# Kernel optimization log

Measured on AMD Instinct MI355X. Metric: run time of the kernel, lower is better.

Reference implementation:

```python
import jax, jax.numpy as jnp
import numpy as np
from jax import lax

B, T, D = 4, 1024, 512      # batch, seq_len, d_model
L = 4                        # n_layers
N = 16                       # d_state
DC = 4                       # d_conv
DI = 2 * D                   # d_inner = expand * d_model
DTR = D // 16                # dt_rank
H = 128                      # head hidden dim
EPS = 1e-5


def layer_norm(x, g, b):
    mu = jnp.mean(x, axis=-1, keepdims=True)
    var = jnp.mean((x - mu) ** 2, axis=-1, keepdims=True)
    return (x - mu) * lax.rsqrt(var + EPS) * g + b


def setup_inputs() -> dict:
    key = jax.random.key(0)
    ks = jax.random.split(key, 24)
    s = 0.02
    return {
        "daily_summaries": jax.random.normal(ks[0], (B, T, D), jnp.float32),
        # per-layer mamba params, stacked on leading L axis
        "in_proj_w": s * jax.random.normal(ks[1], (L, 2 * DI, D), jnp.float32),
        "conv_w": s * jax.random.normal(ks[2], (L, DI, DC), jnp.float32),
        "conv_b": jnp.zeros((L, DI), jnp.float32),
        "x_proj_w": s * jax.random.normal(ks[3], (L, DTR + 2 * N, DI), jnp.float32),
        "dt_proj_w": s * jax.random.normal(ks[4], (L, DI, DTR), jnp.float32),
        "dt_proj_b": jnp.full((L, DI), -4.0, jnp.float32),  # softplus -> small dt
        "A_log": jnp.log(jnp.broadcast_to(jnp.arange(1, N + 1, dtype=jnp.float32), (L, DI, N))),
        "D_skip": jnp.ones((L, DI), jnp.float32),
        "out_proj_w": s * jax.random.normal(ks[5], (L, D, DI), jnp.float32),
        "ln_g": jnp.ones((L, D), jnp.float32),
        "ln_b": jnp.zeros((L, D), jnp.float32),
        # attention pooling
        "attn_w": s * jax.random.normal(ks[6], (1, D), jnp.float32),
        "attn_b": jnp.zeros((1,), jnp.float32),
        # VIX head
        "h1_w": s * jax.random.normal(ks[7], (H, D), jnp.float32),
        "h1_b": jnp.zeros((H,), jnp.float32),
        "ln1_g": jnp.ones((H,), jnp.float32),
        "ln1_b": jnp.zeros((H,), jnp.float32),
        "h2_w": s * jax.random.normal(ks[8], (H, H), jnp.float32),
        "h2_b": jnp.zeros((H,), jnp.float32),
        "ln2_g": jnp.ones((H,), jnp.float32),
        "ln2_b": jnp.zeros((H,), jnp.float32),
        # note: torch zero-inits the final layer; we use random so grads are nonzero
        "h3_w": s * jax.random.normal(ks[9], (1, H), jnp.float32),
        "h3_b": jnp.zeros((1,), jnp.float32),
    }


def mamba_layer(x, in_w, cw, cb, xp_w, dt_w, dt_b, A_log, D_skip, out_w):
    """x: [B,T,D] -> [B,T,D]; canonical Mamba selective scan."""
    xz = jnp.einsum('btd,ed->bte', x, in_w)          # [B,T,2*DI]
    x_in, z = jnp.split(xz, 2, axis=-1)
    # causal depthwise conv over time
    xc = lax.conv_general_dilated(
        x_in.transpose(0, 2, 1), cw[:, None, :], (1,), [(DC - 1, 0)],
        feature_group_count=DI, dimension_numbers=('NCH', 'OIH', 'NCH'))
    xc = jax.nn.silu(xc + cb[None, :, None]).transpose(0, 2, 1)   # [B,T,DI]
    dbc = jnp.einsum('btd,ed->bte', xc, xp_w)        # [B,T,DTR+2N]
    dt_r, Bm, Cm = dbc[..., :DTR], dbc[..., DTR:DTR + N], dbc[..., DTR + N:]
    dt = jax.nn.softplus(jnp.einsum('btr,dr->btd', dt_r, dt_w) + dt_b)  # [B,T,DI]
    A = -jnp.exp(A_log)                              # [DI,N]
    dA = jnp.exp(dt[..., None] * A)                  # [B,T,DI,N]
    dBx = dt[..., None] * Bm[:, :, None, :] * xc[..., None]  # [B,T,DI,N]

    def step(h, inp):
        dA_t, dBx_t, C_t = inp
        h = dA_t * h + dBx_t                         # [B,DI,N]
        return h, jnp.einsum('bdn,bn->bd', h, C_t)

    h0 = jnp.zeros((x.shape[0], DI, N), x.dtype)
    _, ys = lax.scan(step, h0, (dA.transpose(1, 0, 2, 3),
                                dBx.transpose(1, 0, 2, 3),
                                Cm.transpose(1, 0, 2)))
    y = ys.transpose(1, 0, 2) + xc * D_skip          # [B,T,DI]
    y = y * jax.nn.silu(z)
    return jnp.einsum('btd,ed->bte', y, out_w)       # [B,T,D]


def reference(daily_summaries, in_proj_w, conv_w, conv_b, x_proj_w, dt_proj_w,
              dt_proj_b, A_log, D_skip, out_proj_w, ln_g, ln_b, attn_w, attn_b,
              h1_w, h1_b, ln1_g, ln1_b, h2_w, h2_b, ln2_g, ln2_b, h3_w, h3_b):
    x = daily_summaries  # proj is Identity (d_model_l1 == d_model)
    for l in range(L):
        residual = x
        y = mamba_layer(x, in_proj_w[l], conv_w[l], conv_b[l], x_proj_w[l],
                        dt_proj_w[l], dt_proj_b[l], A_log[l], D_skip[l], out_proj_w[l])
        x = layer_norm(y, ln_g[l], ln_b[l]) + residual
    # attention pooling (no mask)
    scores = jnp.einsum('btd,od->bto', x, attn_w) + attn_b   # [B,T,1]
    w = jax.nn.softmax(scores, axis=1)
    pooled = jnp.sum(w * x, axis=1)                          # [B,D]
    # VIX head: Linear -> LN -> GELU (x2) -> Linear
    h1 = jax.nn.gelu(layer_norm(pooled @ h1_w.T + h1_b, ln1_g, ln1_b), approximate=False)
    h2 = jax.nn.gelu(layer_norm(h1 @ h2_w.T + h2_b, ln2_g, ln2_b), approximate=False)
    return (h2 @ h3_w.T + h3_b).squeeze(-1)                  # [B]
```

## Files before the change

kernel.cpp:

```cpp
#include <hip/hip_runtime.h>
#include <hip/hip_bf16.h>
#include <math.h>

#define BATCH 4
#define TLEN 1024
#define DMODEL 512
#define DINNER 1024
#define NSTATE 16
#define EPSV 1e-5f
#define NC 32
#define CT 32
#define DSTR 36
#define LOG2E 1.44269504088896f

typedef __attribute__((ext_vector_type(8))) short bf16x8;
typedef __attribute__((ext_vector_type(4))) float f32x4;

__device__ inline unsigned short f2bf(float f) {
  union { float f; unsigned int u; } c; c.f = f;
  unsigned int u = c.u;
  return (unsigned short)((u + 0x7FFFu + ((u >> 16) & 1u)) >> 16);
}

__device__ inline float warpReduceSum(float v) {
#pragma unroll
  for (int o = 32; o > 0; o >>= 1) v += __shfl_down(v, o, 64);
  return v;
}
__device__ inline float warpReduceMax(float v) {
#pragma unroll
  for (int o = 32; o > 0; o >>= 1) v = fmaxf(v, __shfl_down(v, o, 64));
  return v;
}
__device__ inline float2 blockReduceSum2_256(float a, float b) {
  __shared__ float sma[4], smb[4];
  int lane = threadIdx.x & 63, wid = threadIdx.x >> 6;
#pragma unroll
  for (int o = 32; o > 0; o >>= 1) { a += __shfl_down(a, o, 64); b += __shfl_down(b, o, 64); }
  if (lane == 0) { sma[wid] = a; smb[wid] = b; }
  __syncthreads();
  float ra = sma[0] + sma[1] + sma[2] + sma[3];
  float rb = smb[0] + smb[1] + smb[2] + smb[3];
  __syncthreads();
  return make_float2(ra, rb);
}
__device__ inline float blockReduceSum256(float v) {
  __shared__ float sm[4];
  int lane = threadIdx.x & 63, wid = threadIdx.x >> 6;
  v = warpReduceSum(v);
  if (lane == 0) sm[wid] = v;
  __syncthreads();
  float r = sm[0] + sm[1] + sm[2] + sm[3];
  __syncthreads();
  return r;
}
__device__ inline float blockReduceMax256(float v) {
  __shared__ float sm[4];
  int lane = threadIdx.x & 63, wid = threadIdx.x >> 6;
  v = warpReduceMax(v);
  if (lane == 0) sm[wid] = v;
  __syncthreads();
  float r = fmaxf(fmaxf(sm[0], sm[1]), fmaxf(sm[2], sm[3]));
  __syncthreads();
  return r;
}
__device__ inline float blockReduceSum128(float v) {
  __shared__ float sm[2];
  int lane = threadIdx.x & 63, wid = threadIdx.x >> 6;
  v = warpReduceSum(v);
  if (lane == 0) sm[wid] = v;
  __syncthreads();
  float r = sm[0] + sm[1];
  __syncthreads();
  return r;
}

__global__ void __launch_bounds__(256)
cast_f32_bf16(const float* __restrict__ src, unsigned short* __restrict__ dst, int n) {
  int i = (blockIdx.x * 256 + threadIdx.x) * 4;
  if (i >= n) return;
  float4 v = *(const float4*)(src + i);
  dst[i + 0] = f2bf(v.x);
  dst[i + 1] = f2bf(v.y);
  dst[i + 2] = f2bf(v.z);
  dst[i + 3] = f2bf(v.w);
}

#define LDP 72
__global__ void __launch_bounds__(256)
gemm_bf16(const unsigned short* __restrict__ A, int lda,
          const unsigned short* __restrict__ B, int ldb,
          float* __restrict__ C, int ldc, int K) {
  __shared__ unsigned short As[128 * LDP];
  __shared__ unsigned short Bs[128 * LDP];
  const int tid = threadIdx.x;
  const int lane = tid & 63, wid = tid >> 6;
  const int wm = wid >> 1, wn = wid & 1;
  const int row0 = blockIdx.y * 128, col0 = blockIdx.x * 128;
  const int c8 = (tid & 7) * 8;
  const int r0 = tid >> 3;
  const int l15 = lane & 15, lq = lane >> 4;
  f32x4 acc[4][4] = {};
  for (int k0 = 0; k0 < K; k0 += 64) {
#pragma unroll
    for (int p = 0; p < 4; p++) {
      int row = r0 + p * 32;
      bf16x8 av = *(const bf16x8*)(A + (size_t)(row0 + row) * lda + k0 + c8);
      bf16x8 bv = *(const bf16x8*)(B + (size_t)(col0 + row) * ldb + k0 + c8);
      *(bf16x8*)(As + row * LDP + c8) = av;
      *(bf16x8*)(Bs + row * LDP + c8) = bv;
    }
    __syncthreads();
#pragma unroll
    for (int s = 0; s < 2; s++) {
      const int koff = s * 32 + lq * 8;
      bf16x8 af[4], bfr[4];
#pragma unroll
      for (int i = 0; i < 4; i++)
        af[i] = *(const bf16x8*)(As + (wm * 64 + i * 16 + l15) * LDP + koff);
#pragma unroll
      for (int j = 0; j < 4; j++)
        bfr[j] = *(const bf16x8*)(Bs + (wn * 64 + j * 16 + l15) * LDP + koff);
#pragma unroll
      for (int i = 0; i < 4; i++)
#pragma unroll
        for (int j = 0; j < 4; j++)
          acc[i][j] = __builtin_amdgcn_mfma_f32_16x16x32_bf16(af[i], bfr[j], acc[i][j], 0, 0, 0);
    }
    __syncthreads();
  }
#pragma unroll
  for (int i = 0; i < 4; i++) {
#pragma unroll
    for (int j = 0; j < 4; j++) {
#pragma unroll
      for (int r = 0; r < 4; r++) {
        int row = row0 + wm * 64 + i * 16 + lq * 4 + r;
        int col = col0 + wn * 64 + j * 16 + l15;
        C[(size_t)row * ldc + col] = acc[i][j][r];
      }
    }
  }
}

__global__ void __launch_bounds__(256)
gemm_bf16_n64(const unsigned short* __restrict__ A, int lda,
              const unsigned short* __restrict__ B, int ldb,
              float* __restrict__ C, int ldc, int K) {
  __shared__ unsigned short As[128 * LDP];
  __shared__ unsigned short Bs[64 * LDP];
  const int tid = threadIdx.x;
  const int lane = tid & 63, wid = tid >> 6;
  const int wm = wid >> 1, wn = wid & 1;
  const int row0 = blockIdx.y * 128, col0 = blockIdx.x * 64;
  const int c8 = (tid & 7) * 8;
  const int r0 = tid >> 3;
  const int l15 = lane & 15, lq = lane >> 4;
  f32x4 acc[4][2] = {};
  for (int k0 = 0; k0 < K; k0 += 64) {
#pragma unroll
    for (int p = 0; p < 4; p++) {
      int row = r0 + p * 32;
      bf16x8 av = *(const bf16x8*)(A + (size_t)(row0 + row) * lda + k0 + c8);
      *(bf16x8*)(As + row * LDP + c8) = av;
    }
#pragma unroll
    for (int p = 0; p < 2; p++) {
      int row = r0 + p * 32;
      bf16x8 bv = *(const bf16x8*)(B + (size_t)(col0 + row) * ldb + k0 + c8);
      *(bf16x8*)(Bs + row * LDP + c8) = bv;
    }
    __syncthreads();
#pragma unroll
    for (int s = 0; s < 2; s++) {
      const int koff = s * 32 + lq * 8;
      bf16x8 af[4], bfr[2];
#pragma unroll
      for (int i = 0; i < 4; i++)
        af[i] = *(const bf16x8*)(As + (wm * 64 + i * 16 + l15) * LDP + koff);
#pragma unroll
      for (int j = 0; j < 2; j++)
        bfr[j] = *(const bf16x8*)(Bs + (wn * 32 + j * 16 + l15) * LDP + koff);
#pragma unroll
      for (int i = 0; i < 4; i++)
#pragma unroll
        for (int j = 0; j < 2; j++)
          acc[i][j] = __builtin_amdgcn_mfma_f32_16x16x32_bf16(af[i], bfr[j], acc[i][j], 0, 0, 0);
    }
    __syncthreads();
  }
#pragma unroll
  for (int i = 0; i < 4; i++) {
#pragma unroll
    for (int j = 0; j < 2; j++) {
#pragma unroll
      for (int r = 0; r < 4; r++) {
        int row = row0 + wm * 64 + i * 16 + lq * 4 + r;
        int col = col0 + wn * 32 + j * 16 + l15;
        C[(size_t)row * ldc + col] = acc[i][j][r];
      }
    }
  }
}

template <int EPI>
__global__ void __launch_bounds__(256)
gemm_atb(const float* __restrict__ A, int lda,
         const float* __restrict__ B, int ldb,
         float* __restrict__ C, int ldc,
         int K, const float* __restrict__ bias) {
  __shared__ __align__(16) float As[16][68];
  __shared__ __align__(16) float Bs[16][68];
  const int tid = threadIdx.x;
  const int tx = tid & 15, ty = tid >> 4;
  const int row0 = blockIdx.y * 64, col0 = blockIdx.x * 64;
  float acc[4][4] = {};
  for (int k0 = 0; k0 < K; k0 += 16) {
#pragma unroll
    for (int i = 0; i < 4; i++) {
      int e = tid + i * 256;
      int m = e >> 4, kk = e & 15;
      As[kk][m] = A[(size_t)(row0 + m) * lda + k0 + kk];
      Bs[kk][m] = B[(size_t)(col0 + m) * ldb + k0 + kk];
    }
    __syncthreads();
#pragma unroll
    for (int kk = 0; kk < 16; kk++) {
      float4 a4 = *(const float4*)&As[kk][ty << 2];
      float4 b4 = *(const float4*)&Bs[kk][tx << 2];
      float a[4] = {a4.x, a4.y, a4.z, a4.w};
      float b[4] = {b4.x, b4.y, b4.z, b4.w};
#pragma unroll
      for (int i = 0; i < 4; i++)
#pragma unroll
        for (int j = 0; j < 4; j++) acc[i][j] = fmaf(a[i], b[j], acc[i][j]);
    }
    __syncthreads();
  }
#pragma unroll
  for (int i = 0; i < 4; i++) {
    size_t r = row0 + (ty << 2) + i;
#pragma unroll
    for (int j = 0; j < 4; j++) {
      int c = col0 + (tx << 2) + j;
      float v = acc[i][j];
      if (EPI == 1) {
        v += bias[c];
        v = (v > 20.f) ? v : log1pf(__expf(v));
      }
      C[r * ldc + c] = v;
    }
  }
}

__global__ void __launch_bounds__(256)
gemm_atb_sk(const float* __restrict__ A, int lda,
            const float* __restrict__ B, int ldb,
            float* __restrict__ Cpart, int ldc, int KCH) {
  __shared__ __align__(16) float As[16][68];
  __shared__ __align__(16) float Bs[16][68];
  const int tid = threadIdx.x;
  const int tx = tid & 15, ty = tid >> 4;
  const int row0 = blockIdx.y * 64, col0 = blockIdx.x * 64;
  const int kbase = blockIdx.z * KCH;
  float* Cz = Cpart + (size_t)blockIdx.z * 4096 * 64;
  float acc[4][4] = {};
  for (int k0 = 0; k0 < KCH; k0 += 16) {
#pragma unroll
    for (int i = 0; i < 4; i++) {
      int e = tid + i * 256;
      int m = e >> 4, kk = e & 15;
      As[kk][m] = A[(size_t)(row0 + m) * lda + kbase + k0 + kk];
      Bs[kk][m] = B[(size_t)(col0 + m) * ldb + kbase + k0 + kk];
    }
    __syncthreads();
#pragma unroll
    for (int kk = 0; kk < 16; kk++) {
      float4 a4 = *(const float4*)&As[kk][ty << 2];
      float4 b4 = *(const float4*)&Bs[kk][tx << 2];
      float a[4] = {a4.x, a4.y, a4.z, a4.w};
      float b[4] = {b4.x, b4.y, b4.z, b4.w};
#pragma unroll
      for (int i = 0; i < 4; i++)
#pragma unroll
        for (int j = 0; j < 4; j++) acc[i][j] = fmaf(a[i], b[j], acc[i][j]);
    }
    __syncthreads();
  }
#pragma unroll
  for (int i = 0; i < 4; i++) {
    size_t r = row0 + (ty << 2) + i;
#pragma unroll
    for (int j = 0; j < 4; j++) {
      int c = col0 + (tx << 2) + j;
      Cz[r * ldc + c] = acc[i][j];
    }
  }
}

__global__ void __launch_bounds__(256)
reduce4_kernel(const float* __restrict__ part, float* __restrict__ out, int n) {
  int i = (blockIdx.x * 256 + threadIdx.x) * 4;
  if (i >= n) return;
  float4 a = *(const float4*)(part + i);
  float4 b = *(const float4*)(part + n + i);
  float4 c = *(const float4*)(part + 2 * n + i);
  float4 d = *(const float4*)(part + 3 * n + i);
  float4 r;
  r.x = a.x + b.x + c.x + d.x;
  r.y = a.y + b.y + c.y + d.y;
  r.z = a.z + b.z + c.z + d.z;
  r.w = a.w + b.w + c.w + d.w;
  *(float4*)(out + i) = r;
}

__global__ void conv_silu_kernel(const float* __restrict__ xz,
                                 const float* __restrict__ cw,
                                 const float* __restrict__ cb,
                                 float* __restrict__ xc) {
  int idx = blockIdx.x * 256 + threadIdx.x;
  int d = idx & 1023;
  int bt = idx >> 10;
  int t = bt & 1023;
  float acc = cb[d];
  const float* w = cw + d * 4;
#pragma unroll
  for (int k = 0; k < 4; k++) {
    int ts = t - 3 + k;
    if (ts >= 0) acc = fmaf(xz[((size_t)bt + (ts - t)) * 2048 + d], w[k], acc);
  }
  float sig = 1.f / (1.f + __expf(-acc));
  xc[idx] = acc * sig;
}

__global__ void __launch_bounds__(256)
scan_part1(const float* __restrict__ dt, const float* __restrict__ xc,
           const float* __restrict__ dbc, const float* __restrict__ A_log,
           float* __restrict__ hloc, float* __restrict__ sdtb) {
  __shared__ float dts[64 * DSTR];
  __shared__ float xcs[64 * DSTR];
  __shared__ float Bsh[CT * 20];
  const int chunk = blockIdx.x, dg = blockIdx.y, b = blockIdx.z;
  const int tid = threadIdx.x;
  const int ch = tid >> 2, q4 = (tid & 3) * 4;
  const int d = dg * 64 + ch;
  const size_t bt0 = (size_t)b * TLEN + chunk * CT;
  for (int i = tid; i < CT * 64; i += 256) {
    int t = i >> 6, c = i & 63;
    size_t bt = bt0 + t;
    dts[c * DSTR + t] = dt[bt * 1024 + dg * 64 + c];
    xcs[c * DSTR + t] = xc[bt * 1024 + dg * 64 + c];
  }
  for (int i = tid; i < CT * 16; i += 256) {
    int t = i >> 4, n = i & 15;
    Bsh[t * 20 + n] = dbc[(bt0 + t) * 64 + 32 + n];
  }
  __syncthreads();
  float4 al = *(const float4*)&A_log[d * 16 + q4];
  float4 A;
  A.x = -__expf(al.x) * LOG2E; A.y = -__expf(al.y) * LOG2E;
  A.z = -__expf(al.z) * LOG2E; A.w = -__expf(al.w) * LOG2E;
  float4 h = {0.f, 0.f, 0.f, 0.f};
  float sdt = 0.f;
#pragma unroll
  for (int t0 = 0; t0 < CT; t0 += 4) {
    float4 dt4 = *(const float4*)&dts[ch * DSTR + t0];
    float4 xc4 = *(const float4*)&xcs[ch * DSTR + t0];
    const float dta[4] = {dt4.x, dt4.y, dt4.z, dt4.w};
    const float xca[4] = {xc4.x, xc4.y, xc4.z, xc4.w};
#pragma unroll
    for (int u = 0; u < 4; u++) {
      float dtv = dta[u];
      float4 B4 = *(const float4*)&Bsh[(t0 + u) * 20 + q4];
      float uin = dtv * xca[u];
      h.x = fmaf(exp2f(dtv * A.x), h.x, uin * B4.x);
      h.y = fmaf(exp2f(dtv * A.y), h.y, uin * B4.y);
      h.z = fmaf(exp2f(dtv * A.z), h.z, uin * B4.z);
      h.w = fmaf(exp2f(dtv * A.w), h.w, uin * B4.w);
      sdt += dtv;
    }
  }
  size_t slab = (size_t)(b * 16 + dg);
  *(float4*)&hloc[(slab * NC + chunk) * 1024 + tid * 4] = h;
  sdtb[(slab * NC + chunk) * 256 + tid] = sdt;
}

__global__ void __launch_bounds__(256)
scan_part2(const float* __restrict__ dt, const float* __restrict__ xc,
           const float* __restrict__ dbc, const float* __restrict__ xz,
           const float* __restrict__ A_log, const float* __restrict__ Dsk,
           const float* __restrict__ hloc, const float* __restrict__ sdtb,
           unsigned short* __restrict__ ybf) {
  __shared__ float dts[64 * DSTR];
  __shared__ float xcs[64 * DSTR];
  __shared__ float Bsh[CT * 20];
  __shared__ float Csh[CT * 20];
  __shared__ float ys[CT * 64];
  const int chunk = blockIdx.x, dg = blockIdx.y, b = blockIdx.z;
  const int tid = threadIdx.x;
  const int q = tid & 3;
  const int ch = tid >> 2, q4 = q * 4;
  const int d = dg * 64 + ch;
  const size_t bt0 = (size_t)b * TLEN + chunk * CT;
  float4 al = *(const float4*)&A_log[d * 16 + q4];
  float4 A;
  A.x = -__expf(al.x) * LOG2E; A.y = -__expf(al.y) * LOG2E;
  A.z = -__expf(al.z) * LOG2E; A.w = -__expf(al.w) * LOG2E;
  float4 h = {0.f, 0.f, 0.f, 0.f};
  {
    size_t slab = (size_t)(b * 16 + dg);
    const f32x4* hl4 = (const f32x4*)&hloc[slab * NC * 1024];
    const float* sd = &sdtb[slab * NC * 256 + tid];
    int c = 0;
    for (; c + 4 <= chunk; c += 4) {
      f32x4 hl[4];
      float s[4];
#pragma unroll
      for (int j = 0; j < 4; j++) {
        hl[j] = hl4[(size_t)(c + j) * 256 + tid];
        s[j] = sd[(size_t)(c + j) * 256];
      }
#pragma unroll
      for (int j = 0; j < 4; j++) {
        h.x = fmaf(exp2f(s[j] * A.x), h.x, hl[j][0]);
        h.y = fmaf(exp2f(s[j] * A.y), h.y, hl[j][1]);
        h.z = fmaf(exp2f(s[j] * A.z), h.z, hl[j][2]);
        h.w = fmaf(exp2f(s[j] * A.w), h.w, hl[j][3]);
      }
    }
    for (; c < chunk; c++) {
      f32x4 hl = hl4[(size_t)c * 256 + tid];
      float s = sd[(size_t)c * 256];
      h.x = fmaf(exp2f(s * A.x), h.x, hl[0]);
      h.y = fmaf(exp2f(s * A.y), h.y, hl[1]);
      h.z = fmaf(exp2f(s * A.z), h.z, hl[2]);
      h.w = fmaf(exp2f(s * A.w), h.w, hl[3]);
    }
  }
  for (int i = tid; i < CT * 64; i += 256) {
    int t = i >> 6, c = i & 63;
    size_t bt = bt0 + t;
    dts[c * DSTR + t] = dt[bt * 1024 + dg * 64 + c];
    xcs[c * DSTR + t] = xc[bt * 1024 + dg * 64 + c];
  }
  for (int i = tid; i < CT * 16; i += 256) {
    int t = i >> 4, n = i & 15;
    Bsh[t * 20 + n] = dbc[(bt0 + t) * 64 + 32 + n];
    Csh[t * 20 + n] = dbc[(bt0 + t) * 64 + 48 + n];
  }
  __syncthreads();
  const float Dv = Dsk[d];
#pragma unroll
  for (int t0 = 0; t0 < CT; t0 += 4) {
    float4 dt4 = *(const float4*)&dts[ch * DSTR + t0];
    float4 xc4 = *(const float4*)&xcs[ch * DSTR + t0];
    const float dta[4] = {dt4.x, dt4.y, dt4.z, dt4.w};
    const float xca[4] = {xc4.x, xc4.y, xc4.z, xc4.w};
#pragma unroll
    for (int u = 0; u < 4; u++) {
      float dtv = dta[u];
      float4 B4 = *(const float4*)&Bsh[(t0 + u) * 20 + q4];
      float4 C4 = *(const float4*)&Csh[(t0 + u) * 20 + q4];
      float uin = dtv * xca[u];
      h.x = fmaf(exp2f(dtv * A.x), h.x, uin * B4.x);
      h.y = fmaf(exp2f(dtv * A.y), h.y, uin * B4.y);
      h.z = fmaf(exp2f(dtv * A.z), h.z, uin * B4.z);
      h.w = fmaf(exp2f(dtv * A.w), h.w, uin * B4.w);
      float cs = h.x * C4.x + h.y * C4.y + h.z * C4.z + h.w * C4.w;
      cs += __shfl_xor(cs, 1, 4);
      cs += __shfl_xor(cs, 2, 4);
      if (q == 0) ys[(t0 + u) * 64 + ch] = cs + xca[u] * Dv;
    }
  }
  __syncthreads();
  for (int i = tid; i < CT * 64; i += 256) {
    int t = i >> 6, c = i & 63;
    size_t bt = bt0 + t;
    float zv = xz[bt * 2048 + 1024 + dg * 64 + c];
    float sig = 1.f / (1.f + __expf(-zv));
    ybf[bt * 1024 + dg * 64 + c] = f2bf(ys[t * 64 + c] * (zv * sig));
  }
}

__global__ void __launch_bounds__(256)
ln_res_kernel(const float* __restrict__ mo, const float* __restrict__ res,
              const float* __restrict__ g, const float* __restrict__ bb,
              float* __restrict__ xout, unsigned short* __restrict__ xout_bf) {
  int row = blockIdx.x;
  int tid = threadIdx.x;
  size_t base = (size_t)row * 512;
  float v0 = mo[base + tid], v1 = mo[base + tid + 256];
  float2 ss = blockReduceSum2_256(v0 + v1, v0 * v0 + v1 * v1);
  float mu = ss.x * (1.f / 512.f);
  float var = ss.y * (1.f / 512.f) - mu * mu;
  float rs = rsqrtf(var + EPSV);
  float o0 = (v0 - mu) * rs * g[tid] + bb[tid] + res[base + tid];
  float o1 = (v1 - mu) * rs * g[tid + 256] + bb[tid + 256] + res[base + tid + 256];
  xout[base + tid] = o0;
  xout[base + tid + 256] = o1;
  xout_bf[base + tid] = f2bf(o0);
  xout_bf[base + tid + 256] = f2bf(o1);
}

__global__ void __launch_bounds__(256)
score_kernel(const float* __restrict__ x, const float* __restrict__ aw,
             const float* __restrict__ ab, float* __restrict__ sc) {
  int row = blockIdx.x * 4 + (threadIdx.x >> 6);
  int lane = threadIdx.x & 63;
  size_t base = (size_t)row * 512;
  float p = 0.f;
#pragma unroll
  for (int j = 0; j < 8; j++) p = fmaf(x[base + lane + 64 * j], aw[lane + 64 * j], p);
  p = warpReduceSum(p);
  if (lane == 0) sc[row] = p + ab[0];
}

__global__ void __launch_bounds__(256)
softmax_t_kernel(const float* __restrict__ sc, float* __restrict__ wsm) {
  int b = blockIdx.x, tid = threadIdx.x;
  float v[4];
  float m = -INFINITY;
#pragma unroll
  for (int j = 0; j < 4; j++) { v[j] = sc[b * 1024 + tid + 256 * j]; m = fmaxf(m, v[j]); }
  m = blockReduceMax256(m);
  float s = 0.f;
#pragma unroll
  for (int j = 0; j < 4; j++) { v[j] = __expf(v[j] - m); s += v[j]; }
  s = blockReduceSum256(s);
  float inv = 1.f / s;
#pragma unroll
  for (int j = 0; j < 4; j++) wsm[b * 1024 + tid + 256 * j] = v[j] * inv;
}

__global__ void __launch_bounds__(256)
pool_partial(const float* __restrict__ x, const float* __restrict__ wsm,
             float* __restrict__ partial) {
  int tc = blockIdx.x, b = blockIdx.y, tid = threadIdx.x;
  float a0 = 0.f, a1 = 0.f;
  for (int t = tc * 32; t < tc * 32 + 32; t++) {
    float wv = wsm[b * 1024 + t];
    size_t base = ((size_t)b * 1024 + t) * 512;
    a0 = fmaf(wv, x[base + tid], a0);
    a1 = fmaf(wv, x[base + tid + 256], a1);
  }
  size_t pb = ((size_t)b * 32 + tc) * 512;
  partial[pb + tid] = a0;
  partial[pb + tid + 256] = a1;
}

__global__ void __launch_bounds__(256)
pool_reduce(const float* __restrict__ partial, float* __restrict__ pooled) {
  int b = blockIdx.x, tid = threadIdx.x;
  float a0 = 0.f, a1 = 0.f;
  for (int tc = 0; tc < 32; tc++) {
    size_t pb = ((size_t)b * 32 + tc) * 512;
    a0 += partial[pb + tid];
    a1 += partial[pb + tid + 256];
  }
  pooled[b * 512 + tid] = a0;
  pooled[b * 512 + tid + 256] = a1;
}

__device__ inline float gelu_exact(float x) {
  return 0.5f * x * (1.f + erff(x * 0.70710678118654752f));
}
__global__ void __launch_bounds__(128)
head_kernel(const float* __restrict__ pooled,
            const float* __restrict__ h1w, const float* __restrict__ h1b,
            const float* __restrict__ g1, const float* __restrict__ b1,
            const float* __restrict__ h2w, const float* __restrict__ h2b,
            const float* __restrict__ g2, const float* __restrict__ b2,
            const float* __restrict__ h3w, const float* __restrict__ h3b,
            float* __restrict__ out) {
  int tid = threadIdx.x;
  int b = blockIdx.x;
  __shared__ float hs[128];
  float s = h1b[tid];
  const float* p = pooled + b * 512;
  for (int d = 0; d < 512; d += 4) {
    float4 pv = *(const float4*)(p + d);
    float4 wv = *(const float4*)(h1w + tid * 512 + d);
    s = fmaf(pv.x, wv.x, s); s = fmaf(pv.y, wv.y, s);
    s = fmaf(pv.z, wv.z, s); s = fmaf(pv.w, wv.w, s);
  }
  float mu = blockReduceSum128(s) * (1.f / 128.f);
  float dd = s - mu;
  float var = blockReduceSum128(dd * dd) * (1.f / 128.f);
  float v = dd * rsqrtf(var + EPSV) * g1[tid] + b1[tid];
  hs[tid] = gelu_exact(v);
  __syncthreads();
  float s2 = h2b[tid];
  for (int j = 0; j < 128; j++) s2 = fmaf(hs[j], h2w[tid * 128 + j], s2);
  float mu2 = blockReduceSum128(s2) * (1.f / 128.f);
  float d2 = s2 - mu2;
  float var2 = blockReduceSum128(d2 * d2) * (1.f / 128.f);
  float v2 = d2 * rsqrtf(var2 + EPSV) * g2[tid] + b2[tid];
  float h2v = gelu_exact(v2);
  float o = blockReduceSum128(h2v * h3w[tid]);
  if (tid == 0) out[b] = o + h3b[0];
}

extern "C" void kernel_launch(void* const* d_in, const int* in_sizes, int n_in,
                              void* d_out, int out_size, void* d_ws, size_t ws_size,
                              hipStream_t stream) {
  (void)in_sizes; (void)n_in; (void)out_size; (void)ws_size;
  const float* x0   = (const float*)d_in[0];
  const float* inw  = (const float*)d_in[1];
  const float* cw   = (const float*)d_in[2];
  const float* cb   = (const float*)d_in[3];
  const float* xpw  = (const float*)d_in[4];
  const float* dtw  = (const float*)d_in[5];
  const float* dtb  = (const float*)d_in[6];
  const float* alog = (const float*)d_in[7];
  const float* dsk  = (const float*)d_in[8];
  const float* outw = (const float*)d_in[9];
  const float* lng  = (const float*)d_in[10];
  const float* lnb  = (const float*)d_in[11];
  const float* aw   = (const float*)d_in[12];
  const float* ab   = (const float*)d_in[13];
  const float* h1w  = (const float*)d_in[14];
  const float* h1b  = (const float*)d_in[15];
  const float* g1   = (const float*)d_in[16];
  const float* b1   = (const float*)d_in[17];
  const float* h2w  = (const float*)d_in[18];
  const float* h2b  = (const float*)d_in[19];
  const float* g2   = (const float*)d_in[20];
  const float* b2   = (const float*)d_in[21];
  const float* h3w  = (const float*)d_in[22];
  const float* h3b  = (const float*)d_in[23];

  float* ws = (float*)d_ws;
  float* xz      = ws;
  float* xc      = xz + 8388608;
  float* dbc     = xc + 4194304;
  float* dt      = dbc + 262144;
  float* mo      = dt + 4194304;
  float* xbuf    = mo + 2097152;
  float* scores  = xbuf + 2097152;
  float* wsm     = scores + 4096;
  float* partial = wsm + 4096;
  float* pooled  = partial + 65536;
  unsigned short* abuf    = (unsigned short*)(pooled + 2048);
  unsigned short* ybf     = abuf + 2097152;
  unsigned short* wbf_in  = ybf + 4194304;
  unsigned short* wbf_out = wbf_in + 4194304;
  float* xpart = (float*)(wbf_out + 2097152);
  float* hloc = mo;
  float* sdtb = xpart;

  cast_f32_bf16<<<4096, 256, 0, stream>>>(inw, wbf_in, 4194304);
  cast_f32_bf16<<<2048, 256, 0, stream>>>(outw, wbf_out, 2097152);
  cast_f32_bf16<<<2048, 256, 0, stream>>>(x0, abuf, 2097152);

  const float* xcur = x0;
  for (int l = 0; l < 4; l++) {
    gemm_bf16<<<dim3(16, 32), 256, 0, stream>>>(
        abuf, 512, wbf_in + (size_t)l * 2048 * 512, 512, xz, 2048, 512);
    conv_silu_kernel<<<16384, 256, 0, stream>>>(xz, cw + l * 4096, cb + l * 1024, xc);
    gemm_atb_sk<<<dim3(1, 64, 4), 256, 0, stream>>>(
        xc, 1024, xpw + (size_t)l * 64 * 1024, 1024, xpart, 64, 256);
    reduce4_kernel<<<256, 256, 0, stream>>>(xpart, dbc, 262144);
    gemm_atb<1><<<dim3(16, 64), 256, 0, stream>>>(
        dbc, 64, dtw + (size_t)l * 1024 * 32, 32, dt, 1024, 32, dtb + l * 1024);
    scan_part1<<<dim3(NC, 16, 4), 256, 0, stream>>>(
        dt, xc, dbc, alog + (size_t)l * 16384, hloc, sdtb);
    scan_part2<<<dim3(NC, 16, 4), 256, 0, stream>>>(
        dt, xc, dbc, xz, alog + (size_t)l * 16384, dsk + l * 1024,
        hloc, sdtb, ybf);
    gemm_bf16_n64<<<dim3(8, 32), 256, 0, stream>>>(
        ybf, 1024, wbf_out + (size_t)l * 512 * 1024, 1024, mo, 512, 1024);
    ln_res_kernel<<<4096, 256, 0, stream>>>(mo, xcur, lng + l * 512, lnb + l * 512,
                                            xbuf, abuf);
    xcur = xbuf;
  }
  score_kernel<<<1024, 256, 0, stream>>>(xbuf, aw, ab, scores);
  softmax_t_kernel<<<4, 256, 0, stream>>>(scores, wsm);
  pool_partial<<<dim3(32, 4), 256, 0, stream>>>(xbuf, wsm, partial);
  pool_reduce<<<4, 256, 0, stream>>>(partial, pooled);
  head_kernel<<<4, 128, 0, stream>>>(pooled, h1w, h1b, g1, b1, h2w, h2b, g2, b2,
                                     h3w, h3b, (float*)d_out);
}
```

Baseline: 841.9 us.

## Store intermediates in bf16, MFMA x_proj, and add separate scan prefix kernel

Splits the in_proj output into an fp32 x half and a bf16 z half, and stores conv output and dt in bf16 to cut memory traffic for the scan kernels. The x_proj matmul moves from a split-K fp32 SIMT GEMM plus reduce onto the bf16 MFMA GEMM. A new scan_prefix kernel computes each chunk's initial state once, replacing the redundant per-block serial prefix inside scan_part2. This lowers precision of dt, xc and z to bf16 and adds one launch per layer.

```diff
diff --git a/kernel.cpp b/kernel.cpp
--- a/kernel.cpp
+++ b/kernel.cpp
@@ -21,6 +21,11 @@
   unsigned int u = c.u;
   return (unsigned short)((u + 0x7FFFu + ((u >> 16) & 1u)) >> 16);
 }
+__device__ inline float bf2f(unsigned short u) {
+  union { unsigned int i; float f; } c;
+  c.i = ((unsigned int)u) << 16;
+  return c.f;
+}
 
 __device__ inline float warpReduceSum(float v) {
 #pragma unroll
@@ -88,9 +93,9 @@
 
 #define LDP 72
 __global__ void __launch_bounds__(256)
-gemm_bf16(const unsigned short* __restrict__ A, int lda,
-          const unsigned short* __restrict__ B, int ldb,
-          float* __restrict__ C, int ldc, int K) {
+gemm_bf16_split(const unsigned short* __restrict__ A, int lda,
+                const unsigned short* __restrict__ B, int ldb,
+                float* __restrict__ Cx, unsigned short* __restrict__ Cz, int K) {
   __shared__ unsigned short As[128 * LDP];
   __shared__ unsigned short Bs[128 * LDP];
   const int tid = threadIdx.x;
@@ -129,17 +134,28 @@
     }
     __syncthreads();
   }
-#pragma unroll
-  for (int i = 0; i < 4; i++) {
-#pragma unroll
-    for (int j = 0; j < 4; j++) {
-#pragma unroll
-      for (int r = 0; r < 4; r++) {
-        int row = row0 + wm * 64 + i * 16 + lq * 4 + r;
-        int col = col0 + wn * 64 + j * 16 + l15;
-        C[(size_t)row * ldc + col] = acc[i][j][r];
-      }
-    }
+  if (col0 < 1024) {
+#pragma unroll
+    for (int i = 0; i < 4; i++)
+#pragma unroll
+      for (int j = 0; j < 4; j++)
+#pragma unroll
+        for (int r = 0; r < 4; r++) {
+          int row = row0 + wm * 64 + i * 16 + lq * 4 + r;
+          int col = col0 + wn * 64 + j * 16 + l15;
+          Cx[(size_t)row * 1024 + col] = acc[i][j][r];
+        }
+  } else {
+#pragma unroll
+    for (int i = 0; i < 4; i++)
+#pragma unroll
+      for (int j = 0; j < 4; j++)
+#pragma unroll
+        for (int r = 0; r < 4; r++) {
+          int row = row0 + wm * 64 + i * 16 + lq * 4 + r;
+          int col = col0 - 1024 + wn * 64 + j * 16 + l15;
+          Cz[(size_t)row * 1024 + col] = f2bf(acc[i][j][r]);
+        }
   }
 }
 
@@ -190,38 +206,33 @@
     __syncthreads();
   }
 #pragma unroll
-  for (int i = 0; i < 4; i++) {
-#pragma unroll
-    for (int j = 0; j < 2; j++) {
+  for (int i = 0; i < 4; i++)
+#pragma unroll
+    for (int j = 0; j < 2; j++)
 #pragma unroll
       for (int r = 0; r < 4; r++) {
         int row = row0 + wm * 64 + i * 16 + lq * 4 + r;
         int col = col0 + wn * 32 + j * 16 + l15;
         C[(size_t)row * ldc + col] = acc[i][j][r];
       }
-    }
-  }
-}
-
-template <int EPI>
-__global__ void __launch_bounds__(256)
-gemm_atb(const float* __restrict__ A, int lda,
-         const float* __restrict__ B, int ldb,
-         float* __restrict__ C, int ldc,
-         int K, const float* __restrict__ bias) {
+}
+
+__global__ void __launch_bounds__(256)
+gemm_dt(const float* __restrict__ A, const float* __restrict__ B,
+        unsigned short* __restrict__ C, const float* __restrict__ bias) {
   __shared__ __align__(16) float As[16][68];
   __shared__ __align__(16) float Bs[16][68];
   const int tid = threadIdx.x;
   const int tx = tid & 15, ty = tid >> 4;
   const int row0 = blockIdx.y * 64, col0 = blockIdx.x * 64;
   float acc[4][4] = {};
-  for (int k0 = 0; k0 < K; k0 += 16) {
+  for (int k0 = 0; k0 < 32; k0 += 16) {
 #pragma unroll
     for (int i = 0; i < 4; i++) {
       int e = tid + i * 256;
       int m = e >> 4, kk = e & 15;
-      As[kk][m] = A[(size_t)(row0 + m) * lda + k0 + kk];
-      Bs[kk][m] = B[(size_t)(col0 + m) * ldb + k0 + kk];
+      As[kk][m] = A[(size_t)(row0 + m) * 64 + k0 + kk];
+      Bs[kk][m] = B[(size_t)(col0 + m) * 32 + k0 + kk];
     }
     __syncthreads();
 #pragma unroll
@@ -243,81 +254,17 @@
 #pragma unroll
     for (int j = 0; j < 4; j++) {
       int c = col0 + (tx << 2) + j;
-      float v = acc[i][j];
-      if (EPI == 1) {
-        v += bias[c];
-        v = (v > 20.f) ? v : log1pf(__expf(v));
-      }
-      C[r * ldc + c] = v;
-    }
-  }
-}
-
-__global__ void __launch_bounds__(256)
-gemm_atb_sk(const float* __restrict__ A, int lda,
-            const float* __restrict__ B, int ldb,
-            float* __restrict__ Cpart, int ldc, int KCH) {
-  __shared__ __align__(16) float As[16][68];
-  __shared__ __align__(16) float Bs[16][68];
-  const int tid = threadIdx.x;
-  const int tx = tid & 15, ty = tid >> 4;
-  const int row0 = blockIdx.y * 64, col0 = blockIdx.x * 64;
-  const int kbase = blockIdx.z * KCH;
-  float* Cz = Cpart + (size_t)blockIdx.z * 4096 * 64;
-  float acc[4][4] = {};
-  for (int k0 = 0; k0 < KCH; k0 += 16) {
-#pragma unroll
-    for (int i = 0; i < 4; i++) {
-      int e = tid + i * 256;
-      int m = e >> 4, kk = e & 15;
-      As[kk][m] = A[(size_t)(row0 + m) * lda + kbase + k0 + kk];
-      Bs[kk][m] = B[(size_t)(col0 + m) * ldb + kbase + k0 + kk];
-    }
-    __syncthreads();
-#pragma unroll
-    for (int kk = 0; kk < 16; kk++) {
-      float4 a4 = *(const float4*)&As[kk][ty << 2];
-      float4 b4 = *(const float4*)&Bs[kk][tx << 2];
-      float a[4] = {a4.x, a4.y, a4.z, a4.w};
-      float b[4] = {b4.x, b4.y, b4.z, b4.w};
-#pragma unroll
-      for (int i = 0; i < 4; i++)
-#pragma unroll
-        for (int j = 0; j < 4; j++) acc[i][j] = fmaf(a[i], b[j], acc[i][j]);
-    }
-    __syncthreads();
-  }
-#pragma unroll
-  for (int i = 0; i < 4; i++) {
-    size_t r = row0 + (ty << 2) + i;
-#pragma unroll
-    for (int j = 0; j < 4; j++) {
-      int c = col0 + (tx << 2) + j;
-      Cz[r * ldc + c] = acc[i][j];
-    }
-  }
-}
-
-__global__ void __launch_bounds__(256)
-reduce4_kernel(const float* __restrict__ part, float* __restrict__ out, int n) {
-  int i = (blockIdx.x * 256 + threadIdx.x) * 4;
-  if (i >= n) return;
-  float4 a = *(const float4*)(part + i);
-  float4 b = *(const float4*)(part + n + i);
-  float4 c = *(const float4*)(part + 2 * n + i);
-  float4 d = *(const float4*)(part + 3 * n + i);
-  float4 r;
-  r.x = a.x + b.x + c.x + d.x;
-  r.y = a.y + b.y + c.y + d.y;
-  r.z = a.z + b.z + c.z + d.z;
-  r.w = a.w + b.w + c.w + d.w;
-  *(float4*)(out + i) = r;
-}
-
-__global__ void conv_silu_kernel(const float* __restrict__ xz,
+      float v = acc[i][j] + bias[c];
+      v = (v > 20.f) ? v : log1pf(__expf(v));
+      C[r * 1024 + c] = f2bf(v);
+    }
+  }
+}
+
+__global__ void conv_silu_kernel(const float* __restrict__ xin,
                                  const float* __restrict__ cw,
                                  const float* __restrict__ cb,
-                                 float* __restrict__ xc) {
+                                 unsigned short* __restrict__ xcbf) {
   int idx = blockIdx.x * 256 + threadIdx.x;
   int d = idx & 1023;
   int bt = idx >> 10;
@@ -327,18 +274,18 @@
 #pragma unroll
   for (int k = 0; k < 4; k++) {
     int ts = t - 3 + k;
-    if (ts >= 0) acc = fmaf(xz[((size_t)bt + (ts - t)) * 2048 + d], w[k], acc);
+    if (ts >= 0) acc = fmaf(xin[((size_t)bt + (ts - t)) * 1024 + d], w[k], acc);
   }
   float sig = 1.f / (1.f + __expf(-acc));
-  xc[idx] = acc * sig;
-}
-
-__global__ void __launch_bounds__(256)
-scan_part1(const float* __restrict__ dt, const float* __restrict__ xc,
+  xcbf[idx] = f2bf(acc * sig);
+}
+
+__global__ void __launch_bounds__(256)
+scan_part1(const unsigned short* __restrict__ dtbf, const unsigned short* __restrict__ xcbf,
            const float* __restrict__ dbc, const float* __restrict__ A_log,
            float* __restrict__ hloc, float* __restrict__ sdtb) {
-  __shared__ float dts[64 * DSTR];
-  __shared__ float xcs[64 * DSTR];
+  __shared__ unsigned short dts[64 * DSTR];
+  __shared__ unsigned short xcs[64 * DSTR];
   __shared__ float Bsh[CT * 20];
   const int chunk = blockIdx.x, dg = blockIdx.y, b = blockIdx.z;
   const int tid = threadIdx.x;
@@ -348,8 +295,8 @@
   for (int i = tid; i < CT * 64; i += 256) {
     int t = i >> 6, c = i & 63;
     size_t bt = bt0 + t;
-    dts[c * DSTR + t] = dt[bt * 1024 + dg * 64 + c];
-    xcs[c * DSTR + t] = xc[bt * 1024 + dg * 64 + c];
+    dts[c * DSTR + t] = dtbf[bt * 1024 + dg * 64 + c];
+    xcs[c * DSTR + t] = xcbf[bt * 1024 + dg * 64 + c];
   }
   for (int i = tid; i < CT * 16; i += 256) {
     int t = i >> 4, n = i & 15;
@@ -364,10 +311,10 @@
   float sdt = 0.f;
 #pragma unroll
   for (int t0 = 0; t0 < CT; t0 += 4) {
-    float4 dt4 = *(const float4*)&dts[ch * DSTR + t0];
-    float4 xc4 = *(const float4*)&xcs[ch * DSTR + t0];
-    const float dta[4] = {dt4.x, dt4.y, dt4.z, dt4.w};
-    const float xca[4] = {xc4.x, xc4.y, xc4.z, xc4.w};
+    ushort4 d4 = *(const ushort4*)&dts[ch * DSTR + t0];
+    ushort4 x4 = *(const ushort4*)&xcs[ch * DSTR + t0];
+    const float dta[4] = {bf2f(d4.x), bf2f(d4.y), bf2f(d4.z), bf2f(d4.w)};
+    const float xca[4] = {bf2f(x4.x), bf2f(x4.y), bf2f(x4.z), bf2f(x4.w)};
 #pragma unroll
     for (int u = 0; u < 4; u++) {
       float dtv = dta[u];
@@ -386,13 +333,37 @@
 }
 
 __global__ void __launch_bounds__(256)
-scan_part2(const float* __restrict__ dt, const float* __restrict__ xc,
-           const float* __restrict__ dbc, const float* __restrict__ xz,
+scan_prefix(const float* __restrict__ A_log, const float* __restrict__ hloc,
+            const float* __restrict__ sdtb, float* __restrict__ h0buf) {
+  const int slab = blockIdx.x;
+  const int tid = threadIdx.x;
+  const int dg = slab & 15;
+  const int ch = tid >> 2, q4 = (tid & 3) * 4;
+  const int d = dg * 64 + ch;
+  float4 al = *(const float4*)&A_log[d * 16 + q4];
+  float4 A;
+  A.x = -__expf(al.x) * LOG2E; A.y = -__expf(al.y) * LOG2E;
+  A.z = -__expf(al.z) * LOG2E; A.w = -__expf(al.w) * LOG2E;
+  float4 h = {0.f, 0.f, 0.f, 0.f};
+  size_t base = (size_t)slab * NC;
+  for (int c = 0; c < NC; c++) {
+    *(float4*)&h0buf[(base + c) * 1024 + tid * 4] = h;
+    float4 hl = *(const float4*)&hloc[(base + c) * 1024 + tid * 4];
+    float s = sdtb[(base + c) * 256 + tid];
+    h.x = fmaf(exp2f(s * A.x), h.x, hl.x);
+    h.y = fmaf(exp2f(s * A.y), h.y, hl.y);
+    h.z = fmaf(exp2f(s * A.z), h.z, hl.z);
+    h.w = fmaf(exp2f(s * A.w), h.w, hl.w);
+  }
+}
+
+__global__ void __launch_bounds__(256)
+scan_part2(const unsigned short* __restrict__ dtbf, const unsigned short* __restrict__ xcbf,
+           const float* __restrict__ dbc, const unsigned short* __restrict__ zbf,
            const float* __restrict__ A_log, const float* __restrict__ Dsk,
-           const float* __restrict__ hloc, const float* __restrict__ sdtb,
-           unsigned short* __restrict__ ybf) {
-  __shared__ float dts[64 * DSTR];
-  __shared__ float xcs[64 * DSTR];
+           const float* __restrict__ h0buf, unsigned short* __restrict__ ybf) {
+  __shared__ unsigned short dts[64 * DSTR];
+  __shared__ unsigned short xcs[64 * DSTR];
   __shared__ float Bsh[CT * 20];
   __shared__ float Csh[CT * 20];
   __shared__ float ys[CT * 64];
@@ -402,46 +373,17 @@
   const int ch = tid >> 2, q4 = q * 4;
   const int d = dg * 64 + ch;
   const size_t bt0 = (size_t)b * TLEN + chunk * CT;
+  const size_t slab = (size_t)(b * 16 + dg);
+  float4 h = *(const float4*)&h0buf[(slab * NC + chunk) * 1024 + tid * 4];
   float4 al = *(const float4*)&A_log[d * 16 + q4];
   float4 A;
   A.x = -__expf(al.x) * LOG2E; A.y = -__expf(al.y) * LOG2E;
   A.z = -__expf(al.z) * LOG2E; A.w = -__expf(al.w) * LOG2E;
-  float4 h = {0.f, 0.f, 0.f, 0.f};
-  {
-    size_t slab = (size_t)(b * 16 + dg);
-    const f32x4* hl4 = (const f32x4*)&hloc[slab * NC * 1024];
-    const float* sd = &sdtb[slab * NC * 256 + tid];
-    int c = 0;
-    for (; c + 4 <= chunk; c += 4) {
-      f32x4 hl[4];
-      float s[4];
-#pragma unroll
-      for (int j = 0; j < 4; j++) {
-        hl[j] = hl4[(size_t)(c + j) * 256 + tid];
-        s[j] = sd[(size_t)(c + j) * 256];
-      }
-#pragma unroll
-      for (int j = 0; j < 4; j++) {
-        h.x = fmaf(exp2f(s[j] * A.x), h.x, hl[j][0]);
-        h.y = fmaf(exp2f(s[j] * A.y), h.y, hl[j][1]);
-        h.z = fmaf(exp2f(s[j] * A.z), h.z, hl[j][2]);
-        h.w = fmaf(exp2f(s[j] * A.w), h.w, hl[j][3]);
-      }
-    }
-    for (; c < chunk; c++) {
-      f32x4 hl = hl4[(size_t)c * 256 + tid];
-      float s = sd[(size_t)c * 256];
-      h.x = fmaf(exp2f(s * A.x), h.x, hl[0]);
-      h.y = fmaf(exp2f(s * A.y), h.y, hl[1]);
-      h.z = fmaf(exp2f(s * A.z), h.z, hl[2]);
-      h.w = fmaf(exp2f(s * A.w), h.w, hl[3]);
-    }
-  }
   for (int i = tid; i < CT * 64; i += 256) {
     int t = i >> 6, c = i & 63;
     size_t bt = bt0 + t;
-    dts[c * DSTR + t] = dt[bt * 1024 + dg * 64 + c];
-    xcs[c * DSTR + t] = xc[bt * 1024 + dg * 64 + c];
+    dts[c * DSTR + t] = dtbf[bt * 1024 + dg * 64 + c];
+    xcs[c * DSTR + t] = xcbf[bt * 1024 + dg * 64 + c];
   }
   for (int i = tid; i < CT * 16; i += 256) {
     int t = i >> 4, n = i & 15;
@@ -452,10 +394,10 @@
   const float Dv = Dsk[d];
 #pragma unroll
   for (int t0 = 0; t0 < CT; t0 += 4) {
-    float4 dt4 = *(const float4*)&dts[ch * DSTR + t0];
-    float4 xc4 = *(const float4*)&xcs[ch * DSTR + t0];
-    const float dta[4] = {dt4.x, dt4.y, dt4.z, dt4.w};
-    const float xca[4] = {xc4.x, xc4.y, xc4.z, xc4.w};
+    ushort4 d4 = *(const ushort4*)&dts[ch * DSTR + t0];
+    ushort4 x4 = *(const ushort4*)&xcs[ch * DSTR + t0];
+    const float dta[4] = {bf2f(d4.x), bf2f(d4.y), bf2f(d4.z), bf2f(d4.w)};
+    const float xca[4] = {bf2f(x4.x), bf2f(x4.y), bf2f(x4.z), bf2f(x4.w)};
 #pragma unroll
     for (int u = 0; u < 4; u++) {
       float dtv = dta[u];
@@ -476,7 +418,7 @@
   for (int i = tid; i < CT * 64; i += 256) {
     int t = i >> 6, c = i & 63;
     size_t bt = bt0 + t;
-    float zv = xz[bt * 2048 + 1024 + dg * 64 + c];
+    float zv = bf2f(zbf[bt * 1024 + dg * 64 + c]);
     float sig = 1.f / (1.f + __expf(-zv));
     ybf[bt * 1024 + dg * 64 + c] = f2bf(ys[t * 64 + c] * (zv * sig));
   }
@@ -630,13 +572,17 @@
   const float* h3b  = (const float*)d_in[23];
 
   float* ws = (float*)d_ws;
-  float* xz      = ws;
-  float* xc      = xz + 8388608;
-  float* dbc     = xc + 4194304;
-  float* dt      = dbc + 262144;
-  float* mo      = dt + 4194304;
+  float* xin     = ws;
+  unsigned short* zbf  = (unsigned short*)(xin + 4194304);
+  unsigned short* xcbf = zbf + 4194304;
+  unsigned short* dtbf = xcbf + 4194304;
+  float* dbc     = (float*)(dtbf + 4194304);
+  float* mo      = dbc + 262144;
   float* xbuf    = mo + 2097152;
-  float* scores  = xbuf + 2097152;
+  float* hloc    = xbuf + 2097152;
+  float* sdtb    = hloc + 2097152;
+  float* h0buf   = sdtb + 524288;
+  float* scores  = h0buf + 2097152;
   float* wsm     = scores + 4096;
   float* partial = wsm + 4096;
   float* pooled  = partial + 65536;
@@ -644,31 +590,29 @@
   unsigned short* ybf     = abuf + 2097152;
   unsigned short* wbf_in  = ybf + 4194304;
   unsigned short* wbf_out = wbf_in + 4194304;
-  float* xpart = (float*)(wbf_out + 2097152);
-  float* hloc = mo;
-  float* sdtb = xpart;
+  unsigned short* wbf_xp  = wbf_out + 2097152;
 
   cast_f32_bf16<<<4096, 256, 0, stream>>>(inw, wbf_in, 4194304);
   cast_f32_bf16<<<2048, 256, 0, stream>>>(outw, wbf_out, 2097152);
+  cast_f32_bf16<<<256, 256, 0, stream>>>(xpw, wbf_xp, 262144);
   cast_f32_bf16<<<2048, 256, 0, stream>>>(x0, abuf, 2097152);
 
   const float* xcur = x0;
   for (int l = 0; l < 4; l++) {
-    gemm_bf16<<<dim3(16, 32), 256, 0, stream>>>(
-        abuf, 512, wbf_in + (size_t)l * 2048 * 512, 512, xz, 2048, 512);
-    conv_silu_kernel<<<16384, 256, 0, stream>>>(xz, cw + l * 4096, cb + l * 1024, xc);
-    gemm_atb_sk<<<dim3(1, 64, 4), 256, 0, stream>>>(
-        xc, 1024, xpw + (size_t)l * 64 * 1024, 1024, xpart, 64, 256);
-    reduce4_kernel<<<256, 256, 0, stream>>>(xpart, dbc, 262144);
-    gemm_atb<1><<<dim3(16, 64), 256, 0, stream>>>(
-        dbc, 64, dtw + (size_t)l * 1024 * 32, 32, dt, 1024, 32, dtb + l * 1024);
+    gemm_bf16_split<<<dim3(16, 32), 256, 0, stream>>>(
+        abuf, 512, wbf_in + (size_t)l * 2048 * 512, 512, xin, zbf, 512);
+    conv_silu_kernel<<<16384, 256, 0, stream>>>(xin, cw + l * 4096, cb + l * 1024, xcbf);
+    gemm_bf16_n64<<<dim3(1, 32), 256, 0, stream>>>(
+        xcbf, 1024, wbf_xp + (size_t)l * 65536, 1024, dbc, 64, 1024);
+    gemm_dt<<<dim3(16, 64), 256, 0, stream>>>(
+        dbc, dtw + (size_t)l * 32768, dtbf, dtb + l * 1024);
     scan_part1<<<dim3(NC, 16, 4), 256, 0, stream>>>(
-        dt, xc, dbc, alog + (size_t)l * 16384, hloc, sdtb);
+        dtbf, xcbf, dbc, alog + (size_t)l * 16384, hloc, sdtb);
+    scan_prefix<<<64, 256, 0, stream>>>(alog + (size_t)l * 16384, hloc, sdtb, h0buf);
     scan_part2<<<dim3(NC, 16, 4), 256, 0, stream>>>(
-        dt, xc, dbc, xz, alog + (size_t)l * 16384, dsk + l * 1024,
-        hloc, sdtb, ybf);
+        dtbf, xcbf, dbc, zbf, alog + (size_t)l * 16384, dsk + l * 1024, h0buf, ybf);
     gemm_bf16_n64<<<dim3(8, 32), 256, 0, stream>>>(
-        ybf, 1024, wbf_out + (size_t)l * 512 * 1024, 1024, mo, 512, 1024);
+        ybf, 1024, wbf_out + (size_t)l * 524288, 1024, mo, 512, 1024);
     ln_res_kernel<<<4096, 256, 0, stream>>>(mo, xcur, lng + l * 512, lnb + l * 512,
                                             xbuf, abuf);
     xcur = xbuf;
```

New measurement: 787.4 us. 6.5% less time.
